# Optimization experiments

Measured on AMD Instinct MI355X. Metric: run time of the kernel, lower is better.

## Reference

```python
import jax, jax.numpy as jnp
import numpy as np
import math

B, L, D = 4, 4096, 64

def setup_inputs() -> dict:
    key = jax.random.key(0)
    kq, kk, kv = jax.random.split(key, 3)
    q = jax.random.normal(kq, (B, L, D), dtype=jnp.float32)
    k = jax.random.normal(kk, (B, L, D), dtype=jnp.float32)
    v = jax.random.normal(kv, (B, L, D), dtype=jnp.float32)
    return {"q": q, "k": k, "v": v}

def reference(q, k, v):
    d_model = k.shape[-1]
    # score[b,i,j] = <q_i, k_j> / sqrt(d)   -> [B, L, L]
    score = jnp.einsum('bid,bjd->bij', q, k) / math.sqrt(d_model)
    attn = jax.nn.softmax(score.astype(jnp.float32), axis=-1)
    # Faithful to source: output = (v^T @ attn)^T = attn^T @ v
    # output[b,j,d] = sum_i attn[b,i,j] * v[b,i,d]
    out = jnp.einsum('bij,bid->bjd', attn, v)
    return out
```

## Files before the change

### kernel.cpp

```cpp
#include <hip/hip_runtime.h>
#include <hip/hip_bf16.h>

#define LQ 4096
#define DD 64
#define NB 4
#define NTOT ((size_t)NB * LQ * DD)
#define NROW ((size_t)NB * LQ)

typedef __attribute__((ext_vector_type(4))) float f32x4;
typedef __attribute__((ext_vector_type(8))) short short8;
typedef __attribute__((ext_vector_type(4))) short short4v;
typedef __attribute__((ext_vector_type(2))) unsigned int uint2v;
typedef __attribute__((ext_vector_type(4))) unsigned short ushort4v;

static __device__ __forceinline__ unsigned short f2bf(float x) {
  __hip_bfloat16 h = __float2bfloat16(x);
  return __builtin_bit_cast(unsigned short, h);
}
static __device__ __forceinline__ float bf2f(unsigned short u) {
  unsigned int v = ((unsigned int)u) << 16;
  return __builtin_bit_cast(float, v);
}
static __device__ __forceinline__ float ex2(float x) { return __builtin_amdgcn_exp2f(x); }

static __device__ __forceinline__ f32x4 mfma16(short4v a, short4v b, f32x4 c) {
#if __has_builtin(__builtin_amdgcn_mfma_f32_16x16x16bf16_1k)
  return __builtin_amdgcn_mfma_f32_16x16x16bf16_1k(a, b, c, 0, 0, 0);
#else
  asm volatile("v_mfma_f32_16x16x16_bf16 %0, %1, %2, %0"
               : "+v"(c) : "v"(a), "v"(b));
  return c;
#endif
}

static __device__ __forceinline__ void gl_lds16(const unsigned short* g, unsigned short* l) {
  __builtin_amdgcn_global_load_lds(
      (const __attribute__((address_space(1))) unsigned int*)g,
      (__attribute__((address_space(3))) unsigned int*)l, 16, 0, 0);
}

#define C1 0.18033688011112042f

__global__ __launch_bounds__(256) void prep_kernel(
    const float* __restrict__ q, const float* __restrict__ k,
    const float* __restrict__ v,
    unsigned short* __restrict__ Qb, unsigned short* __restrict__ Kb,
    unsigned short* __restrict__ Vb)
{
  const int arr = blockIdx.x >> 9;
  const size_t off = (((size_t)(blockIdx.x & 511)) * 256 + threadIdx.x) * 8;
  const float* s = arr == 0 ? q : arr == 1 ? k : v;
  unsigned short* d = arr == 0 ? Qb : arr == 1 ? Kb : Vb;
  const f32x4 x0 = *(const f32x4*)(s + off);
  const f32x4 x1 = *(const f32x4*)(s + off + 4);
  ushort4v o0 = { f2bf(x0[0]), f2bf(x0[1]), f2bf(x0[2]), f2bf(x0[3]) };
  ushort4v o1 = { f2bf(x1[0]), f2bf(x1[1]), f2bf(x1[2]), f2bf(x1[3]) };
  *(ushort4v*)(d + off) = o0;
  *(ushort4v*)(d + off + 4) = o1;
}

__global__ __launch_bounds__(256, 2) void stats_kernel(
    const unsigned short* __restrict__ Qb, const unsigned short* __restrict__ Kb,
    float* __restrict__ part_ls)
{
  __shared__ __align__(16) unsigned short stK[3][2048];
  const int bx = blockIdx.x;
  const int jc = bx & 7, it = (bx >> 3) & 15, b = bx >> 7;
  const int tid = threadIdx.x, w = tid >> 6, lane = tid & 63;
  const int l15 = lane & 15, g = lane >> 4;
  const int i0 = it * 256 + w * 64;
  const int jbase = jc * 512;
  const unsigned short* Kbase = Kb + (size_t)b * LQ * DD;

  short8 aq[4][2];
#pragma unroll
  for (int is = 0; is < 4; ++is)
#pragma unroll
    for (int kh = 0; kh < 2; ++kh)
      aq[is][kh] = *(const short8*)(Qb + ((size_t)b * LQ + i0 + is * 16 + l15) * DD + kh * 32 + g * 8);

  float ls[4][4];
#pragma unroll
  for (int is = 0; is < 4; ++is)
#pragma unroll
    for (int qq = 0; qq < 4; ++qq) ls[is][qq] = 0.f;

  const int srow = w * 8 + (lane >> 3);
  const int scol = ((lane & 7) ^ (lane >> 3)) << 3;

  gl_lds16(Kbase + (size_t)(jbase + srow) * DD + scol, &stK[0][w * 512]);
  gl_lds16(Kbase + (size_t)(jbase + 32 + srow) * DD + scol, &stK[1][w * 512]);
  asm volatile("s_waitcnt vmcnt(1)" ::: "memory");
  __builtin_amdgcn_s_barrier();

  for (int itr = 0; itr < 16; ++itr) {
    const int cur = itr % 3;
    const int tn = (itr + 2 < 16) ? itr + 2 : 15;
    gl_lds16(Kbase + (size_t)(jbase + tn * 32 + srow) * DD + scol, &stK[(itr + 2) % 3][w * 512]);

    short8 kf[2][2];
#pragma unroll
    for (int jsub = 0; jsub < 2; ++jsub)
#pragma unroll
      for (int kh = 0; kh < 2; ++kh) {
        const int row = jsub * 16 + l15;
        kf[jsub][kh] = *(const short8*)(&stK[cur][row * 64 + (((kh * 4 + g) ^ (l15 & 7)) << 3)]);
      }
#pragma unroll
    for (int is = 0; is < 4; ++is)
#pragma unroll
      for (int jsub = 0; jsub < 2; ++jsub) {
        f32x4 tt = __builtin_amdgcn_mfma_f32_16x16x32_bf16(
            aq[is][0], kf[jsub][0], (f32x4){0.f, 0.f, 0.f, 0.f}, 0, 0, 0);
        tt = __builtin_amdgcn_mfma_f32_16x16x32_bf16(aq[is][1], kf[jsub][1], tt, 0, 0, 0);
#pragma unroll
        for (int qq = 0; qq < 4; ++qq) ls[is][qq] += ex2(tt[qq] * C1);
      }
    asm volatile("s_waitcnt vmcnt(1)" ::: "memory");
    __builtin_amdgcn_s_barrier();
  }
#pragma unroll
  for (int mask = 1; mask <= 8; mask <<= 1)
#pragma unroll
    for (int is = 0; is < 4; ++is)
#pragma unroll
      for (int qq = 0; qq < 4; ++qq) ls[is][qq] += __shfl_xor(ls[is][qq], mask, 64);
  if (l15 == 0) {
#pragma unroll
    for (int is = 0; is < 4; ++is)
#pragma unroll
      for (int qq = 0; qq < 4; ++qq)
        part_ls[(size_t)jc * NROW + b * LQ + i0 + is * 16 + g * 4 + qq] = ls[is][qq];
  }
}

__global__ __launch_bounds__(256) void combine_kernel(
    const float* __restrict__ part_ls, const unsigned short* __restrict__ Vb,
    unsigned short* __restrict__ Vs)
{
  const size_t base = ((size_t)blockIdx.x * 256 + threadIdx.x) * 8;
  const int r = (int)(base >> 6);
  float l = 0.f;
#pragma unroll
  for (int jc = 0; jc < 8; ++jc) l += part_ls[(size_t)jc * NROW + r];
  const float s = 1.0f / l;
  const ushort4v a = *(const ushort4v*)(Vb + base);
  const ushort4v c = *(const ushort4v*)(Vb + base + 4);
  ushort4v oa = { f2bf(bf2f(a[0]) * s), f2bf(bf2f(a[1]) * s),
                  f2bf(bf2f(a[2]) * s), f2bf(bf2f(a[3]) * s) };
  ushort4v oc = { f2bf(bf2f(c[0]) * s), f2bf(bf2f(c[1]) * s),
                  f2bf(bf2f(c[2]) * s), f2bf(bf2f(c[3]) * s) };
  *(ushort4v*)(Vs + base) = oa;
  *(ushort4v*)(Vs + base + 4) = oc;
}

__global__ __launch_bounds__(1024, 4) void attn_out_kernel(
    const unsigned short* __restrict__ Qb, const unsigned short* __restrict__ Kb,
    const unsigned short* __restrict__ Vs, float* __restrict__ out)
{
  __shared__ __align__(16) unsigned short stage[16][4096];

  const int bx = blockIdx.x;
  const int jt = bx & 63;
  const int b  = bx >> 6;
  const int tid = threadIdx.x, w = tid >> 6, lane = tid & 63;
  const int p = w >> 1, sub = w & 1;
  const int l15 = lane & 15, g = lane >> 4;
  const int j0 = jt * 64 + sub * 32;

  const unsigned short* Qbase = Qb + (size_t)b * LQ * DD;
  const unsigned short* Vbase = Vs + (size_t)b * LQ * DD;

  short8 ka[2][2];
#pragma unroll
  for (int jsl = 0; jsl < 2; ++jsl)
#pragma unroll
    for (int kh = 0; kh < 2; ++kh)
      ka[jsl][kh] = *(const short8*)(Kb + ((size_t)b * LQ + j0 + jsl * 16 + l15) * DD + kh * 32 + g * 8);

  f32x4 acc[2][4];
#pragma unroll
  for (int jsl = 0; jsl < 2; ++jsl)
#pragma unroll
    for (int ds = 0; ds < 4; ++ds) acc[jsl][ds] = (f32x4){0.f, 0.f, 0.f, 0.f};

  const int ibase = p * 512;
  const int qrow = lane >> 3;
  const int qcol = ((lane & 7) ^ (lane >> 3)) << 3;
  const int vgr = ((lane & 31) >> 3) * 4 + ((lane & 7) >> 1);
  const int vdc = (lane >> 5) * 16 + (lane & 1) * 8;

  const unsigned sbyte = (unsigned)(size_t)&stage[w][0];

#define STAGE(I0) do { \
    _Pragma("unroll") \
    for (int kk = 0; kk < 4; ++kk) { \
      gl_lds16(Qbase + (size_t)((I0) + kk * 8 + qrow) * DD + qcol, &stage[w][kk * 512]); \
      gl_lds16(Vbase + (size_t)((I0) + (kk >> 1) * 16 + vgr) * DD + (kk & 1) * 32 + vdc, \
               &stage[w][2048 + kk * 512]); \
    } \
  } while (0)

  STAGE(ibase);
  asm volatile("s_waitcnt vmcnt(0)" ::: "memory");

  for (int itr = 0; itr < 16; ++itr) {
    short8 qf[2][2];
#pragma unroll
    for (int is = 0; is < 2; ++is)
#pragma unroll
      for (int kh = 0; kh < 2; ++kh) {
        const int row = is * 16 + l15;
        qf[is][kh] = *(const short8*)(&stage[w][row * 64 + (((kh * 4 + g) ^ (l15 & 7)) << 3)]);
      }

    unsigned long long v0, v1, v2, v3, v4, v5, v6, v7;
    const unsigned av = sbyte + 4096 + g * 128 + l15 * 8;
    asm volatile(
        "ds_read_b64_tr_b16 %0, %8\n\t"
        "ds_read_b64_tr_b16 %1, %8 offset:512\n\t"
        "ds_read_b64_tr_b16 %2, %8 offset:1024\n\t"
        "ds_read_b64_tr_b16 %3, %8 offset:1536\n\t"
        "ds_read_b64_tr_b16 %4, %8 offset:2048\n\t"
        "ds_read_b64_tr_b16 %5, %8 offset:2560\n\t"
        "ds_read_b64_tr_b16 %6, %8 offset:3072\n\t"
        "ds_read_b64_tr_b16 %7, %8 offset:3584\n\t"
        "s_waitcnt lgkmcnt(0)"
        : "=&v"(v0), "=&v"(v1), "=&v"(v2), "=&v"(v3),
          "=&v"(v4), "=&v"(v5), "=&v"(v6), "=&v"(v7)
        : "v"(av) : "memory");
    short4v vf[2][4];
    vf[0][0] = __builtin_bit_cast(short4v, v0);
    vf[0][1] = __builtin_bit_cast(short4v, v1);
    vf[0][2] = __builtin_bit_cast(short4v, v2);
    vf[0][3] = __builtin_bit_cast(short4v, v3);
    vf[1][0] = __builtin_bit_cast(short4v, v4);
    vf[1][1] = __builtin_bit_cast(short4v, v5);
    vf[1][2] = __builtin_bit_cast(short4v, v6);
    vf[1][3] = __builtin_bit_cast(short4v, v7);

    if (itr + 1 < 16) STAGE(ibase + (itr + 1) * 32);

#pragma unroll
    for (int jsl = 0; jsl < 2; ++jsl) {
      short4v pa[2];
      __builtin_amdgcn_s_setprio(1);
#pragma unroll
      for (int is = 0; is < 2; ++is) {
        f32x4 tt = __builtin_amdgcn_mfma_f32_16x16x32_bf16(
            qf[is][0], ka[jsl][0], (f32x4){0.f, 0.f, 0.f, 0.f}, 0, 0, 0);
        tt = __builtin_amdgcn_mfma_f32_16x16x32_bf16(qf[is][1], ka[jsl][1], tt, 0, 0, 0);
        const unsigned a0 = __builtin_bit_cast(unsigned, ex2(tt[0] * C1)) + 0x8000u;
        const unsigned a1 = __builtin_bit_cast(unsigned, ex2(tt[1] * C1)) + 0x8000u;
        const unsigned a2 = __builtin_bit_cast(unsigned, ex2(tt[2] * C1)) + 0x8000u;
        const unsigned a3 = __builtin_bit_cast(unsigned, ex2(tt[3] * C1)) + 0x8000u;
        uint2v uu;
        uu[0] = __builtin_amdgcn_perm(a1, a0, 0x07060302u);
        uu[1] = __builtin_amdgcn_perm(a3, a2, 0x07060302u);
        pa[is] = __builtin_bit_cast(short4v, uu);
      }
#pragma unroll
      for (int is = 0; is < 2; ++is) {
        acc[jsl][0] = mfma16(pa[is], vf[is][0], acc[jsl][0]);
        acc[jsl][1] = mfma16(pa[is], vf[is][1], acc[jsl][1]);
        acc[jsl][2] = mfma16(pa[is], vf[is][2], acc[jsl][2]);
        acc[jsl][3] = mfma16(pa[is], vf[is][3], acc[jsl][3]);
      }
      __builtin_amdgcn_s_setprio(0);
    }

    asm volatile("s_waitcnt vmcnt(0)" ::: "memory");
  }
#undef STAGE

  __syncthreads();
  float* red = (float*)&stage[0][0];
#pragma unroll
  for (int jsl = 0; jsl < 2; ++jsl)
#pragma unroll
    for (int ds = 0; ds < 4; ++ds)
#pragma unroll
      for (int qq = 0; qq < 4; ++qq)
        red[w * 2048 + (jsl * 16 + g * 4 + qq) * 64 + ds * 16 + l15] = acc[jsl][ds][qq];
  __syncthreads();
  {
    float* op = out + ((size_t)b * LQ + jt * 64) * DD;
#pragma unroll
    for (int rr = 0; rr < 4; ++rr) {
      const int r = w * 4 + rr;
      const int sr = r >> 5, rl = r & 31;
      float s = 0.f;
#pragma unroll
      for (int pp = 0; pp < 8; ++pp)
        s += red[(pp * 2 + sr) * 2048 + rl * 64 + lane];
      op[r * 64 + lane] = s;
    }
  }
}

extern "C" void kernel_launch(void* const* d_in, const int* in_sizes, int n_in,
                              void* d_out, int out_size, void* d_ws, size_t ws_size,
                              hipStream_t stream) {
  const float* q = (const float*)d_in[0];
  const float* k = (const float*)d_in[1];
  const float* v = (const float*)d_in[2];

  unsigned short* Qb = (unsigned short*)d_ws;
  unsigned short* Kb = Qb + NTOT;
  unsigned short* Vb = Kb + NTOT;
  unsigned short* Vs = Vb + NTOT;
  float* part_ls = (float*)(Vs + NTOT);
  float* outp = (float*)d_out;

  prep_kernel<<<1536, 256, 0, stream>>>(q, k, v, Qb, Kb, Vb);
  stats_kernel<<<NB * 16 * 8, 256, 0, stream>>>(Qb, Kb, part_ls);
  combine_kernel<<<512, 256, 0, stream>>>(part_ls, Vb, Vs);
  attn_out_kernel<<<NB * 64, 1024, 0, stream>>>(Qb, Kb, Vs, outp);
}
```

Baseline: 59.73 us.

## Double-buffer per-wave Q/V staging with half-size tiles and deeper prefetch

Splits each wave's LDS staging area into two 16-row buffers. Loads are issued two iterations ahead, and the wait uses vmcnt(4) instead of draining all outstanding loads every iteration. Each iteration now processes 16 query rows instead of 32, so there are twice as many iterations. The aim is to hide global-to-LDS latency behind MFMA work, at the cost of more loop overhead and less work per wait.

```diff
diff --git a/kernel.cpp b/kernel.cpp
--- a/kernel.cpp
+++ b/kernel.cpp
@@ -158,7 +158,7 @@
     const unsigned short* __restrict__ Qb, const unsigned short* __restrict__ Kb,
     const unsigned short* __restrict__ Vs, float* __restrict__ out)
 {
-  __shared__ __align__(16) unsigned short stage[16][4096];
+  __shared__ __align__(16) unsigned short stage[16][2][2048];
 
   const int bx = blockIdx.x;
   const int jt = bx & 63;
@@ -187,94 +187,75 @@
   const int ibase = p * 512;
   const int qrow = lane >> 3;
   const int qcol = ((lane & 7) ^ (lane >> 3)) << 3;
-  const int vgr = ((lane & 31) >> 3) * 4 + ((lane & 7) >> 1);
+  const int vgr = ((lane & 31) >> 3) * 4 + ((lane >> 1) & 3);
   const int vdc = (lane >> 5) * 16 + (lane & 1) * 8;
 
-  const unsigned sbyte = (unsigned)(size_t)&stage[w][0];
-
-#define STAGE(I0) do { \
+  const unsigned sbyte = (unsigned)(size_t)&stage[w][0][0];
+
+#define STAGE(BUF, I0) do { \
     _Pragma("unroll") \
-    for (int kk = 0; kk < 4; ++kk) { \
-      gl_lds16(Qbase + (size_t)((I0) + kk * 8 + qrow) * DD + qcol, &stage[w][kk * 512]); \
-      gl_lds16(Vbase + (size_t)((I0) + (kk >> 1) * 16 + vgr) * DD + (kk & 1) * 32 + vdc, \
-               &stage[w][2048 + kk * 512]); \
+    for (int kk = 0; kk < 2; ++kk) { \
+      gl_lds16(Qbase + (size_t)((I0) + kk * 8 + qrow) * DD + qcol, &stage[w][BUF][kk * 512]); \
+      gl_lds16(Vbase + (size_t)((I0) + vgr) * DD + kk * 32 + vdc, &stage[w][BUF][1024 + kk * 512]); \
     } \
   } while (0)
 
-  STAGE(ibase);
-  asm volatile("s_waitcnt vmcnt(0)" ::: "memory");
-
-  for (int itr = 0; itr < 16; ++itr) {
-    short8 qf[2][2];
-#pragma unroll
-    for (int is = 0; is < 2; ++is)
-#pragma unroll
-      for (int kh = 0; kh < 2; ++kh) {
-        const int row = is * 16 + l15;
-        qf[is][kh] = *(const short8*)(&stage[w][row * 64 + (((kh * 4 + g) ^ (l15 & 7)) << 3)]);
-      }
-
-    unsigned long long v0, v1, v2, v3, v4, v5, v6, v7;
-    const unsigned av = sbyte + 4096 + g * 128 + l15 * 8;
+  STAGE(0, ibase);
+  STAGE(1, ibase + 16);
+
+  for (int itr = 0; itr < 32; ++itr) {
+    const int cur = itr & 1;
+    if (itr < 31) asm volatile("s_waitcnt vmcnt(4)" ::: "memory");
+    else          asm volatile("s_waitcnt vmcnt(0)" ::: "memory");
+
+    short8 qf[2];
+#pragma unroll
+    for (int kh = 0; kh < 2; ++kh)
+      qf[kh] = *(const short8*)(&stage[w][cur][l15 * 64 + (((kh * 4 + g) ^ (l15 & 7)) << 3)]);
+
+    unsigned long long v0, v1, v2, v3;
+    const unsigned av = sbyte + cur * 4096 + 2048 + g * 128 + l15 * 8;
     asm volatile(
-        "ds_read_b64_tr_b16 %0, %8\n\t"
-        "ds_read_b64_tr_b16 %1, %8 offset:512\n\t"
-        "ds_read_b64_tr_b16 %2, %8 offset:1024\n\t"
-        "ds_read_b64_tr_b16 %3, %8 offset:1536\n\t"
-        "ds_read_b64_tr_b16 %4, %8 offset:2048\n\t"
-        "ds_read_b64_tr_b16 %5, %8 offset:2560\n\t"
-        "ds_read_b64_tr_b16 %6, %8 offset:3072\n\t"
-        "ds_read_b64_tr_b16 %7, %8 offset:3584\n\t"
+        "ds_read_b64_tr_b16 %0, %4\n\t"
+        "ds_read_b64_tr_b16 %1, %4 offset:512\n\t"
+        "ds_read_b64_tr_b16 %2, %4 offset:1024\n\t"
+        "ds_read_b64_tr_b16 %3, %4 offset:1536\n\t"
         "s_waitcnt lgkmcnt(0)"
-        : "=&v"(v0), "=&v"(v1), "=&v"(v2), "=&v"(v3),
-          "=&v"(v4), "=&v"(v5), "=&v"(v6), "=&v"(v7)
+        : "=&v"(v0), "=&v"(v1), "=&v"(v2), "=&v"(v3)
         : "v"(av) : "memory");
-    short4v vf[2][4];
-    vf[0][0] = __builtin_bit_cast(short4v, v0);
-    vf[0][1] = __builtin_bit_cast(short4v, v1);
-    vf[0][2] = __builtin_bit_cast(short4v, v2);
-    vf[0][3] = __builtin_bit_cast(short4v, v3);
-    vf[1][0] = __builtin_bit_cast(short4v, v4);
-    vf[1][1] = __builtin_bit_cast(short4v, v5);
-    vf[1][2] = __builtin_bit_cast(short4v, v6);
-    vf[1][3] = __builtin_bit_cast(short4v, v7);
-
-    if (itr + 1 < 16) STAGE(ibase + (itr + 1) * 32);
-
+    short4v vf[4];
+    vf[0] = __builtin_bit_cast(short4v, v0);
+    vf[1] = __builtin_bit_cast(short4v, v1);
+    vf[2] = __builtin_bit_cast(short4v, v2);
+    vf[3] = __builtin_bit_cast(short4v, v3);
+
+    if (itr + 2 < 32) STAGE(cur, ibase + (itr + 2) * 16);
+
+    __builtin_amdgcn_s_setprio(1);
 #pragma unroll
     for (int jsl = 0; jsl < 2; ++jsl) {
-      short4v pa[2];
-      __builtin_amdgcn_s_setprio(1);
-#pragma unroll
-      for (int is = 0; is < 2; ++is) {
-        f32x4 tt = __builtin_amdgcn_mfma_f32_16x16x32_bf16(
-            qf[is][0], ka[jsl][0], (f32x4){0.f, 0.f, 0.f, 0.f}, 0, 0, 0);
-        tt = __builtin_amdgcn_mfma_f32_16x16x32_bf16(qf[is][1], ka[jsl][1], tt, 0, 0, 0);
-        const unsigned a0 = __builtin_bit_cast(unsigned, ex2(tt[0] * C1)) + 0x8000u;
-        const unsigned a1 = __builtin_bit_cast(unsigned, ex2(tt[1] * C1)) + 0x8000u;
-        const unsigned a2 = __builtin_bit_cast(unsigned, ex2(tt[2] * C1)) + 0x8000u;
-        const unsigned a3 = __builtin_bit_cast(unsigned, ex2(tt[3] * C1)) + 0x8000u;
-        uint2v uu;
-        uu[0] = __builtin_amdgcn_perm(a1, a0, 0x07060302u);
-        uu[1] = __builtin_amdgcn_perm(a3, a2, 0x07060302u);
-        pa[is] = __builtin_bit_cast(short4v, uu);
-      }
-#pragma unroll
-      for (int is = 0; is < 2; ++is) {
-        acc[jsl][0] = mfma16(pa[is], vf[is][0], acc[jsl][0]);
-        acc[jsl][1] = mfma16(pa[is], vf[is][1], acc[jsl][1]);
-        acc[jsl][2] = mfma16(pa[is], vf[is][2], acc[jsl][2]);
-        acc[jsl][3] = mfma16(pa[is], vf[is][3], acc[jsl][3]);
-      }
-      __builtin_amdgcn_s_setprio(0);
+      f32x4 tt = __builtin_amdgcn_mfma_f32_16x16x32_bf16(
+          qf[0], ka[jsl][0], (f32x4){0.f, 0.f, 0.f, 0.f}, 0, 0, 0);
+      tt = __builtin_amdgcn_mfma_f32_16x16x32_bf16(qf[1], ka[jsl][1], tt, 0, 0, 0);
+      const unsigned a0 = __builtin_bit_cast(unsigned, ex2(tt[0] * C1)) + 0x8000u;
+      const unsigned a1 = __builtin_bit_cast(unsigned, ex2(tt[1] * C1)) + 0x8000u;
+      const unsigned a2 = __builtin_bit_cast(unsigned, ex2(tt[2] * C1)) + 0x8000u;
+      const unsigned a3 = __builtin_bit_cast(unsigned, ex2(tt[3] * C1)) + 0x8000u;
+      uint2v uu;
+      uu[0] = __builtin_amdgcn_perm(a1, a0, 0x07060302u);
+      uu[1] = __builtin_amdgcn_perm(a3, a2, 0x07060302u);
+      const short4v pa = __builtin_bit_cast(short4v, uu);
+      acc[jsl][0] = mfma16(pa, vf[0], acc[jsl][0]);
+      acc[jsl][1] = mfma16(pa, vf[1], acc[jsl][1]);
+      acc[jsl][2] = mfma16(pa, vf[2], acc[jsl][2]);
+      acc[jsl][3] = mfma16(pa, vf[3], acc[jsl][3]);
     }
-
-    asm volatile("s_waitcnt vmcnt(0)" ::: "memory");
+    __builtin_amdgcn_s_setprio(0);
   }
 #undef STAGE
 
   __syncthreads();
-  float* red = (float*)&stage[0][0];
+  float* red = (float*)&stage[0][0][0];
 #pragma unroll
   for (int jsl = 0; jsl < 2; ++jsl)
 #pragma unroll
```

Result: no change. 60.80 us (median of 2 runs) (+1.8%).
